# Kernel optimization log

Measured on AMD Instinct MI355X. Metric: run time of the kernel, lower is better.

Reference implementation:

```python
import jax, jax.numpy as jnp
import numpy as np

B, N, T, F_IN = 16, 1024, 12, 1
D_MODEL, D_K, D_V, H, K = 512, 32, 32, 3, 3
C = 32  # nb_chev_filter == nb_time_filter


def _ln(x, g, b, eps=1e-5):
    mu = jnp.mean(x, -1, keepdims=True)
    var = jnp.var(x, -1, keepdims=True)
    return (x - mu) * jax.lax.rsqrt(var + eps) * g + b


def _conv(x, w, b):
    y = jax.lax.conv_general_dilated(x, w, (1, 1), 'VALID',
                                     dimension_numbers=('NCHW', 'OIHW', 'NCHW'))
    return y + b[None, :, None, None]


def setup_inputs() -> dict:
    key = jax.random.key(0)
    ks = iter(jax.random.split(key, 40))
    rn = lambda s, sc=0.02: jax.random.normal(next(ks), s, jnp.float32) * sc
    return dict(
        x=rn((B, N, F_IN, T), 1.0),
        res_att=rn((B, F_IN, H, T, T), 0.1),
        pos_embed_T=rn((T, N)),
        gamma_T=jnp.ones((N,)), beta_T=jnp.zeros((N,)),
        WQ_t=rn((N, D_K * H)), WK_t=rn((N, D_K * H)), WV_t=rn((N, D_V * H)),
        fc_t=rn((H * D_V, N)),
        pre_conv_w=rn((D_MODEL, T, 1, F_IN)), pre_conv_b=rn((D_MODEL,)),
        pos_embed_S=rn((N, D_MODEL)),
        gamma_S=jnp.ones((D_MODEL,)), beta_S=jnp.zeros((D_MODEL,)),
        WQ_s=rn((D_MODEL, D_K * K)), WK_s=rn((D_MODEL, D_K * K)),
        cheb_polys=rn((K, N, N), 0.05),
        adj_pa=(jax.random.uniform(next(ks), (N, N)) < 0.01).astype(jnp.float32),
        cheb_mask=rn((K, N, N)),
        Theta=rn((K, F_IN, C), 0.1),
        gtu3_w=rn((2 * C, C, 1, 3)), gtu3_b=rn((2 * C,)),
        gtu5_w=rn((2 * C, C, 1, 5)), gtu5_b=rn((2 * C,)),
        gtu7_w=rn((2 * C, C, 1, 7)), gtu7_b=rn((2 * C,)),
        res_conv_w=rn((C, F_IN, 1, 1)), res_conv_b=rn((C,)),
        fcmy_w=rn((3 * T - 12, T)), fcmy_b=rn((T,)),
        gamma_f=jnp.ones((C,)), beta_f=jnp.zeros((C,)),
    )


def reference(x, res_att, pos_embed_T, gamma_T, beta_T, WQ_t, WK_t, WV_t, fc_t,
              pre_conv_w, pre_conv_b, pos_embed_S, gamma_S, beta_S, WQ_s, WK_s,
              cheb_polys, adj_pa, cheb_mask, Theta,
              gtu3_w, gtu3_b, gtu5_w, gtu5_b, gtu7_w, gtu7_b,
              res_conv_w, res_conv_b, fcmy_w, fcmy_b, gamma_f, beta_f):
    B_, N_, F_, T_ = x.shape
    # ---- temporal embedding (num_of_features == 1 branch): (B,F,T,N) ----
    TEmx = _ln(jnp.transpose(x, (0, 2, 3, 1)) + pos_embed_T[None, None], gamma_T, beta_T)

    # ---- temporal MHA with residual attention bias ----
    def heads(e, W, d):
        y = e @ W  # (B,F,T,H*d)
        return jnp.transpose(y.reshape(B_, F_, T_, H, d), (0, 1, 3, 2, 4))  # (B,F,H,T,d)
    Q, Kt, V = heads(TEmx, WQ_t, D_K), heads(TEmx, WK_t, D_K), heads(TEmx, WV_t, D_V)
    re_At = jnp.einsum('bfhqd,bfhkd->bfhqk', Q, Kt) / np.sqrt(D_K) + res_att
    attn = jax.nn.softmax(re_At, axis=-1)
    ctx = jnp.einsum('bfhqk,bfhkd->bfhqd', attn, V)
    ctx = jnp.transpose(ctx, (0, 1, 3, 2, 4)).reshape(B_, F_, T_, H * D_V)
    one_n, zero_n = jnp.ones((N_,), x.dtype), jnp.zeros((N_,), x.dtype)
    TATout = _ln(ctx @ fc_t + TEmx, one_n, zero_n)  # fresh LayerNorm(d_model) -> gamma=1, beta=0

    # ---- pre_conv: Conv2d(T, d_model, kernel=(1,F)) on (B,T,N,F); take last col ----
    x_TAt = jnp.einsum('btnf,dtf->bnd', jnp.transpose(TATout, (0, 2, 3, 1)),
                       pre_conv_w[:, :, 0, :]) + pre_conv_b  # (B,N,d_model)

    # ---- spatial embedding + spatial attention scores (no softmax) ----
    SEmx = _ln(x_TAt + pos_embed_S[None], gamma_S, beta_S)  # dropout = identity (eval)
    Qs = jnp.transpose((SEmx @ WQ_s).reshape(B_, N_, K, D_K), (0, 2, 1, 3))
    Ks = jnp.transpose((SEmx @ WK_s).reshape(B_, N_, K, D_K), (0, 2, 1, 3))
    STAt = jnp.einsum('bknd,bkmd->bknm', Qs, Ks) / np.sqrt(D_K)  # (B,K,N,N)

    # ---- Chebyshev graph conv weighted by spatial attention ----
    satt = jax.nn.softmax(STAt + (adj_pa[None] * cheb_mask)[None], axis=2)
    Tka = cheb_polys[None] * satt  # (B,K,N,N)
    rhs = jnp.einsum('bkmn,bmft->bknft', Tka, x)  # T_k_with_at^T @ x over all t
    spatial_gcn = jax.nn.relu(jnp.einsum('bknft,kfo->bnot', rhs, Theta))  # (B,N,C,T)

    # ---- gated temporal convs (GTU) ----
    X = jnp.transpose(spatial_gcn, (0, 2, 1, 3))  # (B,C,N,T)
    def gtu(w, b):
        y = _conv(X, w, b)
        return jnp.tanh(y[:, :C]) * jax.nn.sigmoid(y[:, C:])
    time_conv = jnp.concatenate([gtu(gtu3_w, gtu3_b), gtu(gtu5_w, gtu5_b),
                                 gtu(gtu7_w, gtu7_b)], axis=-1)  # (B,C,N,3T-12)
    time_conv = time_conv @ fcmy_w + fcmy_b  # (B,C,N,T)
    tco = jax.nn.relu(time_conv)  # num_of_features == 1 branch

    # ---- residual 1x1 conv + final LayerNorm over channel dim ----
    x_res = _conv(jnp.transpose(x, (0, 2, 1, 3)), res_conv_w, res_conv_b)  # (B,C,N,T)
    out = _ln(jnp.transpose(jax.nn.relu(x_res + tco), (0, 3, 2, 1)), gamma_f, beta_f)
    out = jnp.transpose(out, (0, 2, 3, 1))  # (B,N,C,T)
    return out, re_At
```

## Files before the change

### kernel.cpp

```cpp
#include <hip/hip_runtime.h>
#include <hip/hip_bf16.h>
#include <math.h>

#define B_ 16
#define N_ 1024
#define T_ 12
#define DM_ 512
#define H_ 3
#define K_ 3
#define C_ 32
#define RSQRT_DK 0.17677669529663687f

typedef __attribute__((ext_vector_type(8))) short bf16x8;
typedef __attribute__((ext_vector_type(4))) float f32x4;

__device__ __forceinline__ ushort f2bf(float f) {
  uint u = __float_as_uint(f);
  return (ushort)((u + 0x7FFF + ((u >> 16) & 1)) >> 16);
}
__device__ __forceinline__ float bf2f(ushort h) {
  return __uint_as_float(((uint)h) << 16);
}

__global__ void k1_temporal_ln(const float* __restrict__ x, const float* __restrict__ posT,
                               const float* __restrict__ gT, const float* __restrict__ bT,
                               float* __restrict__ TEmx) {
  int row = blockIdx.x;
  int b = row / T_, t = row - b * T_;
  __shared__ float red[256], red2[256];
  float v[4]; float s = 0.f, s2 = 0.f;
  for (int i = 0; i < 4; ++i) {
    int n = threadIdx.x + (i << 8);
    float val = x[(b * N_ + n) * T_ + t] + posT[t * N_ + n];
    v[i] = val; s += val; s2 += val * val;
  }
  red[threadIdx.x] = s; red2[threadIdx.x] = s2;
  __syncthreads();
  for (int off = 128; off > 0; off >>= 1) {
    if (threadIdx.x < off) { red[threadIdx.x] += red[threadIdx.x + off]; red2[threadIdx.x] += red2[threadIdx.x + off]; }
    __syncthreads();
  }
  float mu = red[0] * (1.f / N_);
  float rs = rsqrtf(red2[0] * (1.f / N_) - mu * mu + 1e-5f);
  for (int i = 0; i < 4; ++i) {
    int n = threadIdx.x + (i << 8);
    TEmx[row * N_ + n] = (v[i] - mu) * rs * gT[n] + bT[n];
  }
}

__global__ __launch_bounds__(256) void k2_qkv(const float* __restrict__ TEmx,
                       const float* __restrict__ WQ, const float* __restrict__ WK,
                       const float* __restrict__ WV, float* __restrict__ part) {
  int kc = blockIdx.x, row = blockIdx.y;
  __shared__ float e[256];
  int tid = threadIdx.x;
  e[tid] = TEmx[row * N_ + kc * 256 + tid];
  __syncthreads();
  for (int col = tid; col < 288; col += 256) {
    int which = col / 96, j = col - which * 96;
    const float* W = (which == 0) ? WQ : ((which == 1) ? WK : WV);
    const float* Wp = W + (size_t)(kc * 256) * 96 + j;
    float acc = 0.f;
    #pragma unroll 8
    for (int n = 0; n < 256; ++n) acc += e[n] * Wp[n * 96];
    part[(row * 4 + kc) * 288 + col] = acc;
  }
}

__global__ void k3a_attn(const float* __restrict__ part, const float* __restrict__ res_att,
                         float* __restrict__ reAt_out, float* __restrict__ ctx) {
  int b = blockIdx.x;
  __shared__ float q_l[T_ * 288];
  __shared__ float s_l[H_ * T_ * T_];
  for (int i = threadIdx.x; i < T_ * 288; i += 256) {
    int t = i / 288, col = i - t * 288;
    const float* pr = &part[(size_t)((b * T_ + t) * 4) * 288 + col];
    q_l[i] = pr[0] + pr[288] + pr[576] + pr[864];
  }
  __syncthreads();
  for (int idx = threadIdx.x; idx < H_ * T_ * T_; idx += 256) {
    int h = idx / 144, r = idx - h * 144, qi = r / 12, ki = r - qi * 12;
    float acc = 0.f;
    #pragma unroll
    for (int d = 0; d < 32; ++d)
      acc += q_l[qi * 288 + h * 32 + d] * q_l[ki * 288 + 96 + h * 32 + d];
    float sv = acc * RSQRT_DK + res_att[(b * H_ + h) * 144 + qi * 12 + ki];
    s_l[idx] = sv;
    reAt_out[(b * H_ + h) * 144 + qi * 12 + ki] = sv;
  }
  __syncthreads();
  if (threadIdx.x < 36) {
    int h = threadIdx.x / 12, qi = threadIdx.x - h * 12;
    float mx = -1e30f;
    for (int ki = 0; ki < 12; ++ki) mx = fmaxf(mx, s_l[h * 144 + qi * 12 + ki]);
    float sum = 0.f;
    for (int ki = 0; ki < 12; ++ki) { float p = __expf(s_l[h * 144 + qi * 12 + ki] - mx); s_l[h * 144 + qi * 12 + ki] = p; sum += p; }
    float inv = 1.f / sum;
    for (int ki = 0; ki < 12; ++ki) s_l[h * 144 + qi * 12 + ki] *= inv;
  }
  __syncthreads();
  for (int idx = threadIdx.x; idx < T_ * 96; idx += 256) {
    int qi = idx / 96, hd = idx - qi * 96, h = hd >> 5, d = hd & 31;
    float acc = 0.f;
    for (int ki = 0; ki < 12; ++ki)
      acc += s_l[h * 144 + qi * 12 + ki] * q_l[ki * 288 + 192 + h * 32 + d];
    ctx[(b * T_ + qi) * 96 + hd] = acc;
  }
}

__global__ __launch_bounds__(1024) void k3b_tat(const float* __restrict__ ctx,
                        const float* __restrict__ fc_t,
                        const float* __restrict__ TEmx, float* __restrict__ TAT) {
  int row = blockIdx.x;
  __shared__ float c_l[96];
  __shared__ float red[16], red2[16];
  int tid = threadIdx.x;
  if (tid < 96) c_l[tid] = ctx[row * 96 + tid];
  __syncthreads();
  float acc = TEmx[row * N_ + tid];
  #pragma unroll 12
  for (int j = 0; j < 96; ++j) acc = fmaf(c_l[j], fc_t[j * N_ + tid], acc);
  float s = acc, s2 = acc * acc;
  #pragma unroll
  for (int off = 32; off > 0; off >>= 1) {
    s  += __shfl_xor(s, off);
    s2 += __shfl_xor(s2, off);
  }
  int w = tid >> 6;
  if ((tid & 63) == 0) { red[w] = s; red2[w] = s2; }
  __syncthreads();
  float ts = 0.f, ts2 = 0.f;
  #pragma unroll
  for (int i = 0; i < 16; ++i) { ts += red[i]; ts2 += red2[i]; }
  float mu = ts * (1.f / N_);
  float rs = rsqrtf(ts2 * (1.f / N_) - mu * mu + 1e-5f);
  TAT[row * N_ + tid] = (acc - mu) * rs;
}

__global__ __launch_bounds__(256) void k4_preconv_ln(const float* __restrict__ TAT, const float* __restrict__ pcw,
                              const float* __restrict__ pcb, const float* __restrict__ posS,
                              const float* __restrict__ gS, const float* __restrict__ bS,
                              float* __restrict__ SEmx) {
  int wid = blockIdx.x * 4 + (threadIdx.x >> 6);
  int b = wid >> 10, n = wid & 1023;
  int lane = threadIdx.x & 63;
  float tc[12];
  #pragma unroll
  for (int t = 0; t < 12; ++t) tc[t] = TAT[(b * T_ + t) * N_ + n];
  float v[8]; float s = 0.f, s2 = 0.f;
  #pragma unroll
  for (int i = 0; i < 8; ++i) {
    int d = lane + (i << 6);
    const float4* pw = (const float4*)&pcw[d * 12];
    float4 w0 = pw[0], w1 = pw[1], w2 = pw[2];
    float acc = pcb[d];
    acc += tc[0] * w0.x + tc[1] * w0.y + tc[2] * w0.z + tc[3] * w0.w;
    acc += tc[4] * w1.x + tc[5] * w1.y + tc[6] * w1.z + tc[7] * w1.w;
    acc += tc[8] * w2.x + tc[9] * w2.y + tc[10] * w2.z + tc[11] * w2.w;
    acc += posS[(size_t)n * DM_ + d];
    v[i] = acc; s += acc; s2 += acc * acc;
  }
  #pragma unroll
  for (int off = 1; off < 64; off <<= 1) {
    s  += __shfl_xor(s, off);
    s2 += __shfl_xor(s2, off);
  }
  float mu = s * (1.f / DM_);
  float rs = rsqrtf(s2 * (1.f / DM_) - mu * mu + 1e-5f);
  #pragma unroll
  for (int i = 0; i < 8; ++i) {
    int d = lane + (i << 6);
    SEmx[(size_t)wid * DM_ + d] = (v[i] - mu) * rs * gS[d] + bS[d];
  }
}

__global__ void k5_pre(const float* __restrict__ WQs, const float* __restrict__ WKs,
                       ushort* __restrict__ wpre) {
  int idx = blockIdx.x * 256 + threadIdx.x;
  int k = idx / 192, col = idx - k * 192;
  float v = (col < 96) ? WQs[k * 96 + col] : WKs[k * 96 + (col - 96)];
  wpre[col * 512 + k] = f2bf(v);
}

__global__ __launch_bounds__(256) void k5_qks(const float* __restrict__ SEmx,
                                              const ushort* __restrict__ wpre,
                                              __hip_bfloat16* __restrict__ Qs,
                                              __hip_bfloat16* __restrict__ Ks) {
  int b = blockIdx.y, n0 = blockIdx.x * 32;
  __shared__ __align__(16) ushort SE_h[32 * 520];
  int tid = threadIdx.x;
  for (int idx = tid; idx < 4096; idx += 256) {
    int r = idx >> 7, cq = idx & 127;
    float4 v = *(const float4*)&SEmx[((size_t)((b << 10) + n0 + r)) * DM_ + cq * 4];
    uint lo = (uint)f2bf(v.x) | ((uint)f2bf(v.y) << 16);
    uint hi = (uint)f2bf(v.z) | ((uint)f2bf(v.w) << 16);
    *(uint2*)&SE_h[r * 520 + cq * 4] = make_uint2(lo, hi);
  }
  __syncthreads();

  int w = tid >> 6, lane = tid & 63, quad = lane >> 4, c16 = lane & 15;
  f32x4 acc[3][2];
  #pragma unroll
  for (int mi = 0; mi < 3; ++mi)
    #pragma unroll
    for (int nt = 0; nt < 2; ++nt) acc[mi][nt] = (f32x4){0.f, 0.f, 0.f, 0.f};

  for (int ks = 0; ks < 16; ++ks) {
    bf16x8 Bf0 = *(const bf16x8*)&SE_h[(0 * 16 + c16) * 520 + ks * 32 + quad * 8];
    bf16x8 Bf1 = *(const bf16x8*)&SE_h[(1 * 16 + c16) * 520 + ks * 32 + quad * 8];
    #pragma unroll
    for (int mi = 0; mi < 3; ++mi) {
      int m = (w * 3 + mi) * 16 + c16;
      bf16x8 Af = *(const bf16x8*)&wpre[m * 512 + ks * 32 + quad * 8];
      acc[mi][0] = __builtin_amdgcn_mfma_f32_16x16x32_bf16(Af, Bf0, acc[mi][0], 0, 0, 0);
      acc[mi][1] = __builtin_amdgcn_mfma_f32_16x16x32_bf16(Af, Bf1, acc[mi][1], 0, 0, 0);
    }
  }
  #pragma unroll
  for (int mi = 0; mi < 3; ++mi) {
    int mb = (w * 3 + mi) * 16;
    #pragma unroll
    for (int nt = 0; nt < 2; ++nt) {
      int node = n0 + nt * 16 + c16;
      #pragma unroll
      for (int r = 0; r < 4; ++r) {
        int m = mb + quad * 4 + r;
        int j = (m < 96) ? m : m - 96;
        int kk = j >> 5, dd = j & 31;
        __hip_bfloat16* o = (m < 96) ? Qs : Ks;
        o[(((b * K_ + kk) * N_) + node) * 32 + dd] = __float2bfloat16(acc[mi][nt][r]);
      }
    }
  }
}

__global__ void k6_pre(const float* __restrict__ adj, const float* __restrict__ mask,
                       const float* __restrict__ cheb, uint* __restrict__ pk) {
  int idx = blockIdx.x * 256 + threadIdx.x;
  int mn = idx & (N_ * N_ - 1);
  uint lo = f2bf(adj[mn] * mask[idx]);
  uint hi = f2bf(cheb[idx]);
  pk[idx] = lo | (hi << 16);
}

__global__ __launch_bounds__(256) void k6_spatial(
    const __hip_bfloat16* __restrict__ Qs, const __hip_bfloat16* __restrict__ Ks,
    const uint* __restrict__ pk, const float* __restrict__ x,
    float* __restrict__ rhs) {
  const int b  = blockIdx.x;
  const int k  = blockIdx.y;
  const int n0 = blockIdx.z * 32;
  const ushort* Qb = (const ushort*)(Qs + (size_t)((b * K_ + k) * N_) * 32);
  const ushort* Kb = (const ushort*)(Ks + (size_t)((b * K_ + k) * N_) * 32);
  const uint* pkk = pk + (size_t)k * (N_ * N_);
  const float* xb = x + b * N_ * T_;

  __shared__ float wmu[4][32], well[4][32];
  __shared__ float wacc[4][32][12];

  const int tid  = threadIdx.x;
  const int w    = tid >> 6, lane = tid & 63;
  const int quad = lane >> 4, c16 = lane & 15;

  bf16x8 bfr0 = *(const bf16x8*)(Kb + (size_t)(n0 + c16) * 32 + quad * 8);
  bf16x8 bfr1 = *(const bf16x8*)(Kb + (size_t)(n0 + 16 + c16) * 32 + quad * 8);

  float mu0 = -1e30f, mu1 = -1e30f, el0 = 0.f, el1 = 0.f;
  float acc0[12], acc1[12];
  #pragma unroll
  for (int t = 0; t < 12; ++t) { acc0[t] = 0.f; acc1[t] = 0.f; }

  for (int s = 0; s < 16; ++s) {
    const int m0 = s * 64 + w * 16;
    bf16x8 af = *(const bf16x8*)(Qb + (size_t)(m0 + c16) * 32 + quad * 8);
    f32x4 z = {0.f, 0.f, 0.f, 0.f};
    f32x4 sc0 = __builtin_amdgcn_mfma_f32_16x16x32_bf16(af, bfr0, z, 0, 0, 0);
    f32x4 sc1 = __builtin_amdgcn_mfma_f32_16x16x32_bf16(af, bfr1, z, 0, 0, 0);

    const int mrow = m0 + quad * 4;
    float sv0[4], sv1[4], ch0[4], ch1[4];
    #pragma unroll
    for (int r = 0; r < 4; ++r) {
      uint p2 = pkk[(size_t)(mrow + r) * N_ + n0 + c16];
      uint q2 = pkk[(size_t)(mrow + r) * N_ + n0 + 16 + c16];
      sv0[r] = sc0[r] * RSQRT_DK + __uint_as_float(p2 << 16);
      ch0[r] = __uint_as_float(p2 & 0xFFFF0000u);
      sv1[r] = sc1[r] * RSQRT_DK + __uint_as_float(q2 << 16);
      ch1[r] = __uint_as_float(q2 & 0xFFFF0000u);
    }
    float cm0 = fmaxf(fmaxf(sv0[0], sv0[1]), fmaxf(sv0[2], sv0[3]));
    float cm1 = fmaxf(fmaxf(sv1[0], sv1[1]), fmaxf(sv1[2], sv1[3]));
    cm0 = fmaxf(cm0, __shfl_xor(cm0, 16)); cm0 = fmaxf(cm0, __shfl_xor(cm0, 32));
    cm1 = fmaxf(cm1, __shfl_xor(cm1, 16)); cm1 = fmaxf(cm1, __shfl_xor(cm1, 32));
    float nm0 = fmaxf(mu0, cm0), nm1 = fmaxf(mu1, cm1);
    float f0 = __expf(mu0 - nm0), f1 = __expf(mu1 - nm1);
    mu0 = nm0; mu1 = nm1;
    el0 *= f0; el1 *= f1;
    #pragma unroll
    for (int t = 0; t < 12; ++t) { acc0[t] *= f0; acc1[t] *= f1; }

    float p0[4], p1[4];
    #pragma unroll
    for (int r = 0; r < 4; ++r) {
      p0[r] = __expf(sv0[r] - mu0); el0 += p0[r]; p0[r] *= ch0[r];
      p1[r] = __expf(sv1[r] - mu1); el1 += p1[r]; p1[r] *= ch1[r];
    }
    #pragma unroll
    for (int r = 0; r < 4; ++r) {
      const float4* xr = (const float4*)(xb + (size_t)(mrow + r) * 12);
      float4 xA = xr[0], xB = xr[1], xC = xr[2];
      float xv[12] = {xA.x, xA.y, xA.z, xA.w, xB.x, xB.y, xB.z, xB.w,
                      xC.x, xC.y, xC.z, xC.w};
      float px0 = p0[r], px1 = p1[r];
      #pragma unroll
      for (int t = 0; t < 12; ++t) {
        acc0[t] = fmaf(px0, xv[t], acc0[t]);
        acc1[t] = fmaf(px1, xv[t], acc1[t]);
      }
    }
  }

  #pragma unroll
  for (int off = 16; off <= 32; off <<= 1) {
    el0 += __shfl_xor(el0, off);
    el1 += __shfl_xor(el1, off);
    #pragma unroll
    for (int t = 0; t < 12; ++t) {
      acc0[t] += __shfl_xor(acc0[t], off);
      acc1[t] += __shfl_xor(acc1[t], off);
    }
  }
  if (quad == 0) {
    wmu[w][c16] = mu0; well[w][c16] = el0;
    #pragma unroll
    for (int t = 0; t < 12; ++t) wacc[w][c16][t] = acc0[t];
  } else if (quad == 1) {
    wmu[w][16 + c16] = mu1; well[w][16 + c16] = el1;
    #pragma unroll
    for (int t = 0; t < 12; ++t) wacc[w][16 + c16][t] = acc1[t];
  }
  __syncthreads();
  if (tid < 384) {
    int n = tid / 12, t = tid - n * 12;
    float m0v = wmu[0][n], m1v = wmu[1][n], m2v = wmu[2][n], m3v = wmu[3][n];
    float gm = fmaxf(fmaxf(m0v, m1v), fmaxf(m2v, m3v));
    float e0 = __expf(m0v - gm), e1 = __expf(m1v - gm);
    float e2 = __expf(m2v - gm), e3 = __expf(m3v - gm);
    float den = well[0][n] * e0 + well[1][n] * e1 + well[2][n] * e2 + well[3][n] * e3;
    float num = wacc[0][n][t] * e0 + wacc[1][n][t] * e1 +
                wacc[2][n][t] * e2 + wacc[3][n][t] * e3;
    rhs[((size_t)(b * K_ + k) * N_ + n0 + n) * 12 + t] = num / den;
  }
}

template<int KS, int JV, int JB>
__device__ __forceinline__ void conv_mfma(const ushort* X_th, const ushort* wl_h,
                                          ushort* tc_h, const float* bias0,
                                          int mp, int ntg, int quad, int c16) {
  f32x4 accA[3], accB[3];
  #pragma unroll
  for (int i = 0; i < 3; ++i) { accA[i] = (f32x4){0.f,0.f,0.f,0.f}; accB[i] = (f32x4){0.f,0.f,0.f,0.f}; }
  #pragma unroll
  for (int dt = 0; dt < KS; ++dt) {
    bf16x8 A0 = *(const bf16x8*)&wl_h[dt * 2560 + (mp * 16 + c16) * 40 + quad * 8];
    bf16x8 A1 = *(const bf16x8*)&wl_h[dt * 2560 + ((mp + 2) * 16 + c16) * 40 + quad * 8];
    #pragma unroll
    for (int i = 0; i < 3; ++i) {
      int nt = ntg * 3 + i;
      int j = nt >> 1, sh = nt & 1;
      if (j < JV) {
        bf16x8 Bf = *(const bf16x8*)&X_th[(sh * 16 + c16) * 584 + (j + dt) * 32 + quad * 8];
        accA[i] = __builtin_amdgcn_mfma_f32_16x16x32_bf16(A0, Bf, accA[i], 0, 0, 0);
        accB[i] = __builtin_amdgcn_mfma_f32_16x16x32_bf16(A1, Bf, accB[i], 0, 0, 0);
      }
    }
  }
  #pragma unroll
  for (int i = 0; i < 3; ++i) {
    int nt = ntg * 3 + i, j = nt >> 1, sh = nt & 1;
    if (j < JV) {
      int s = sh * 16 + c16;
      #pragma unroll
      for (int r = 0; r < 4; ++r) {
        int cc = mp * 16 + quad * 4 + r;
        int sx = ((s & 15) << 1) ^ ((cc & 4) << 3) ^ ((cc & 8) >> 1);
        float a = accA[i][r] + bias0[cc];
        float g = accB[i][r] + bias0[cc + 32];
        float e2a = __expf(2.f * a);
        float th = 1.f - 2.f / (e2a + 1.f);
        float sg = 1.f / (1.f + __expf(-g));
        tc_h[((s * 32 + cc) * 32 + (JB + j)) ^ sx] = f2bf(th * sg);
      }
    }
  }
}

__global__ __launch_bounds__(1024) void k8_fused(
                       const float* __restrict__ rhs, const float* __restrict__ Theta,
                       const float* __restrict__ x, const float* __restrict__ rw,
                       const float* __restrict__ rb,
                       const float* __restrict__ w3, const float* __restrict__ b3,
                       const float* __restrict__ w5, const float* __restrict__ b5,
                       const float* __restrict__ w7, const float* __restrict__ b7,
                       const float* __restrict__ fw, const float* __restrict__ fb,
                       const float* __restrict__ gf, const float* __restrict__ bf,
                       float* __restrict__ out) {
  int bn0 = blockIdx.x * 32;
  int b = bn0 >> 10, n0 = bn0 & 1023;

  __shared__ __align__(16) char uR[73216];
  ushort* X_th = (ushort*)uR;
  ushort* wl_h = (ushort*)(uR + 37376);
  float*  v_l  = (float*)uR;
  __shared__ __align__(16) ushort tc_h[1024 * 32];
  __shared__ float rhs_l[32 * 36];
  __shared__ float Th_l[96];
  __shared__ float xr_l[32 * 12];
  __shared__ float fw_l[288];
  __shared__ float fb_l[12];
  __shared__ float bias_l[3][64];
  __shared__ float rw_l[32], rb_l[32], gf_l[32], bf_l[32];
  __shared__ float stm[384], str[384];

  int tid = threadIdx.x;
  int w = tid >> 6, lane = tid & 63, quad = lane >> 4, c16 = lane & 15;
  int mp = w & 1, ntg = w >> 1;
  int c = (tid >> 3) & 31;
  int site = (tid & 7) | ((tid >> 8) << 3);

  for (int idx = tid; idx < 1152; idx += 1024) {
    int s = idx / 36, r = idx - s * 36, k = r / 12, t = r - k * 12;
    rhs_l[idx] = rhs[((size_t)(b * 3 + k) * N_ + n0 + s) * 12 + t];
  }
  if (tid < 384) xr_l[tid] = x[(size_t)(b * N_ + n0) * 12 + tid];
  if (tid < 96) Th_l[tid] = Theta[tid];
  if (tid < 288) fw_l[tid] = fw[tid];
  if (tid < 12) fb_l[tid] = fb[tid];
  if (tid < 64) { bias_l[0][tid] = b3[tid]; bias_l[1][tid] = b5[tid]; bias_l[2][tid] = b7[tid]; }
  if (tid >= 64 && tid < 96)  rw_l[tid - 64] = rw[tid - 64];
  if (tid >= 96 && tid < 128) rb_l[tid - 96] = rb[tid - 96];
  if (tid >= 128 && tid < 160) gf_l[tid - 128] = gf[tid - 128];
  if (tid >= 160 && tid < 192) bf_l[tid - 160] = bf[tid - 160];
  for (int idx = tid; idx < 64 * 32 * 3; idx += 1024) {
    int co = idx / 96, r2 = idx - co * 96, ic = r2 / 3, dt = r2 - ic * 3;
    wl_h[dt * 2560 + co * 40 + ic] = f2bf(w3[idx]);
  }
  __syncthreads();

  {
    float th0 = Th_l[c], th1 = Th_l[32 + c], th2 = Th_l[64 + c];
    const float* rs_ = &rhs_l[site * 36];
    ushort* xo = &X_th[site * 584 + c];
    #pragma unroll
    for (int t = 0; t < 12; ++t) {
      float a = rs_[t] * th0 + rs_[12 + t] * th1 + rs_[24 + t] * th2;
      xo[t * 32] = f2bf(fmaxf(a, 0.f));
    }
  }
  for (int idx = tid; idx < 32 * 6 * 32; idx += 1024) {
    int s = idx / 192, r2 = idx - s * 192, tt = r2 >> 5, ic = r2 & 31;
    X_th[s * 584 + (12 + tt) * 32 + ic] = 0;
  }
  __syncthreads();

  conv_mfma<3, 10, 0>(X_th, wl_h, tc_h, &bias_l[0][0], mp, ntg, quad, c16);
  __syncthreads();
  for (int idx = tid; idx < 64 * 32 * 5; idx += 1024) {
    int co = idx / 160, r2 = idx - co * 160, ic = r2 / 5, dt = r2 - ic * 5;
    wl_h[dt * 2560 + co * 40 + ic] = f2bf(w5[idx]);
  }
  __syncthreads();
  conv_mfma<5, 8, 10>(X_th, wl_h, tc_h, &bias_l[1][0], mp, ntg, quad, c16);
  __syncthreads();
  for (int idx = tid; idx < 64 * 32 * 7; idx += 1024) {
    int co = idx / 224, r2 = idx - co * 224, ic = r2 / 7, dt = r2 - ic * 7;
    wl_h[dt * 2560 + co * 40 + ic] = f2bf(w7[idx]);
  }
  __syncthreads();
  conv_mfma<7, 6, 18>(X_th, wl_h, tc_h, &bias_l[2][0], mp, ntg, quad, c16);
  __syncthreads();

  float tcv[24];
  {
    int rb2 = (site * 32 + c) * 32;
    int sxr = ((site & 15) << 1) ^ ((c & 4) << 3) ^ ((c & 8) >> 1);
    #pragma unroll
    for (int j = 0; j < 24; ++j)
      tcv[j] = __uint_as_float(((uint)tc_h[(rb2 + j) ^ sxr]) << 16);
  }
  float o[12];
  #pragma unroll
  for (int t = 0; t < 12; ++t) o[t] = fb_l[t];
  #pragma unroll
  for (int j = 0; j < 24; ++j) {
    const float4* fp = (const float4*)&fw_l[j * 12];
    float4 f0 = fp[0], f1 = fp[1], f2 = fp[2];
    float fr[12] = {f0.x, f0.y, f0.z, f0.w, f1.x, f1.y, f1.z, f1.w, f2.x, f2.y, f2.z, f2.w};
    #pragma unroll
    for (int t = 0; t < 12; ++t) o[t] = fmaf(tcv[j], fr[t], o[t]);
  }

  float v[12];
  {
    float rwc = rw_l[c], rbc = rb_l[c];
    const float* xs = &xr_l[site * 12];
    float* vo = &v_l[site * 391 + c * 12];
    #pragma unroll
    for (int t = 0; t < 12; ++t) {
      float xres = xs[t] * rwc + rbc;
      v[t] = fmaxf(xres + fmaxf(o[t], 0.f), 0.f);
      vo[t] = v[t];
    }
  }
  __syncthreads();
  if (tid < 384) {
    int s = tid / 12, t = tid - s * 12;
    float sm = 0.f, s2 = 0.f;
    #pragma unroll 8
    for (int cc = 0; cc < 32; ++cc) {
      float u = v_l[s * 391 + cc * 12 + t];
      sm += u; s2 += u * u;
    }
    float m = sm * (1.f / 32.f);
    stm[tid] = m;
    str[tid] = rsqrtf(s2 * (1.f / 32.f) - m * m + 1e-5f);
  }
  __syncthreads();
  {
    float gfc = gf_l[c], bfc = bf_l[c];
    const float* sm_ = &stm[site * 12];
    const float* sr_ = &str[site * 12];
    float q[12];
    #pragma unroll
    for (int t = 0; t < 12; ++t) q[t] = (v[t] - sm_[t]) * sr_[t] * gfc + bfc;
    float* op = &out[(size_t)(bn0 + site) * 384 + c * 12];
    ((float4*)op)[0] = make_float4(q[0], q[1], q[2], q[3]);
    ((float4*)op)[1] = make_float4(q[4], q[5], q[6], q[7]);
    ((float4*)op)[2] = make_float4(q[8], q[9], q[10], q[11]);
  }
}

extern "C" void kernel_launch(void* const* d_in, const int* in_sizes, int n_in,
                              void* d_out, int out_size, void* d_ws, size_t ws_size,
                              hipStream_t stream) {
  const float* x       = (const float*)d_in[0];
  const float* res_att = (const float*)d_in[1];
  const float* posT    = (const float*)d_in[2];
  const float* gT      = (const float*)d_in[3];
  const float* bT      = (const float*)d_in[4];
  const float* WQt     = (const float*)d_in[5];
  const float* WKt     = (const float*)d_in[6];
  const float* WVt     = (const float*)d_in[7];
  const float* fct     = (const float*)d_in[8];
  const float* pcw     = (const float*)d_in[9];
  const float* pcb     = (const float*)d_in[10];
  const float* posS    = (const float*)d_in[11];
  const float* gS      = (const float*)d_in[12];
  const float* bS      = (const float*)d_in[13];
  const float* WQs     = (const float*)d_in[14];
  const float* WKs     = (const float*)d_in[15];
  const float* cheb    = (const float*)d_in[16];
  const float* adj     = (const float*)d_in[17];
  const float* mask    = (const float*)d_in[18];
  const float* Theta   = (const float*)d_in[19];
  const float* w3      = (const float*)d_in[20];
  const float* b3      = (const float*)d_in[21];
  const float* w5      = (const float*)d_in[22];
  const float* b5      = (const float*)d_in[23];
  const float* w7      = (const float*)d_in[24];
  const float* b7      = (const float*)d_in[25];
  const float* rw      = (const float*)d_in[26];
  const float* rb      = (const float*)d_in[27];
  const float* fw      = (const float*)d_in[28];
  const float* fb      = (const float*)d_in[29];
  const float* gf      = (const float*)d_in[30];
  const float* bf      = (const float*)d_in[31];

  float* ws = (float*)d_ws;
  float* TEmx = ws;
  float* qkv  = TEmx + 196608;
  float* ctx  = qkv + 55296;
  float* TAT  = ctx + 18432;
  float* SEmx = TAT + 196608;
  float* Qsf  = SEmx + 8388608;
  float* Ksf  = Qsf + 1572864;
  float* rhs  = Ksf + 1572864;
  ushort* wpre = (ushort*)(rhs + 589824);
  float* part = SEmx;

  __hip_bfloat16* Qh = (__hip_bfloat16*)Qsf;
  __hip_bfloat16* Kh = (__hip_bfloat16*)Ksf;
  uint* pk = (uint*)SEmx;

  float* out  = (float*)d_out;
  float* reAt = out + 6291456;

  k5_pre<<<(DM_ * 192) / 256, 256, 0, stream>>>(WQs, WKs, wpre);
  k1_temporal_ln<<<B_ * T_, 256, 0, stream>>>(x, posT, gT, bT, TEmx);
  k2_qkv<<<dim3(4, B_ * T_), 256, 0, stream>>>(TEmx, WQt, WKt, WVt, part);
  k3a_attn<<<B_, 256, 0, stream>>>(part, res_att, reAt, ctx);
  k3b_tat<<<B_ * T_, 1024, 0, stream>>>(ctx, fct, TEmx, TAT);
  k4_preconv_ln<<<B_ * N_ / 4, 256, 0, stream>>>(TAT, pcw, pcb, posS, gS, bS, SEmx);
  k5_qks<<<dim3(N_ / 32, B_), 256, 0, stream>>>(SEmx, wpre, Qh, Kh);
  k6_pre<<<(K_ * N_ * N_) / 256, 256, 0, stream>>>(adj, mask, cheb, pk);
  k6_spatial<<<dim3(B_, K_, N_ / 32), 256, 0, stream>>>(Qh, Kh, pk, x, rhs);
  k8_fused<<<B_ * N_ / 32, 1024, 0, stream>>>(rhs, Theta, x, rw, rb,
                                              w3, b3, w5, b5, w7, b7, fw, fb, gf, bf, out);
}
```

Before: 363.7 us.

## Precompute bf16 GTU conv weights globally and split temporal attention per head

A new k8_pre kernel converts the three GTU conv weight tensors to bf16 once, in MFMA-friendly layout, into an unused workspace slot. k8_fused then loads the A fragments straight from global memory instead of converting and staging weights in LDS before each conv. This removes the per-block conversion loops and several barriers, and shrinks the shared-memory buffer. The cost is weight fetches through the cache hierarchy inside the MFMA loop. Separately, k3a_attn now runs one block per (batch, head), launching three times as many blocks with smaller LDS tiles.

Result: faster. 329.2 us (-9.5%).

```diff
diff --git a/kernel.cpp b/kernel.cpp
--- a/kernel.cpp
+++ b/kernel.cpp
@@ -67,44 +67,46 @@
   }
 }
 
-__global__ void k3a_attn(const float* __restrict__ part, const float* __restrict__ res_att,
+__global__ __launch_bounds__(256) void k3a_attn(const float* __restrict__ part, const float* __restrict__ res_att,
                          float* __restrict__ reAt_out, float* __restrict__ ctx) {
-  int b = blockIdx.x;
-  __shared__ float q_l[T_ * 288];
-  __shared__ float s_l[H_ * T_ * T_];
-  for (int i = threadIdx.x; i < T_ * 288; i += 256) {
-    int t = i / 288, col = i - t * 288;
+  int bh = blockIdx.x;
+  int b = bh / 3, h = bh - b * 3;
+  __shared__ float q_l[3 * T_ * 32];
+  __shared__ float s_l[T_ * T_];
+  int tid = threadIdx.x;
+  for (int i = tid; i < 1152; i += 256) {
+    int sec = i / 384, r = i - sec * 384, t = r >> 5, d = r & 31;
+    int col = sec * 96 + h * 32 + d;
     const float* pr = &part[(size_t)((b * T_ + t) * 4) * 288 + col];
     q_l[i] = pr[0] + pr[288] + pr[576] + pr[864];
   }
   __syncthreads();
-  for (int idx = threadIdx.x; idx < H_ * T_ * T_; idx += 256) {
-    int h = idx / 144, r = idx - h * 144, qi = r / 12, ki = r - qi * 12;
+  if (tid < 144) {
+    int qi = tid / 12, ki = tid - qi * 12;
     float acc = 0.f;
     #pragma unroll
     for (int d = 0; d < 32; ++d)
-      acc += q_l[qi * 288 + h * 32 + d] * q_l[ki * 288 + 96 + h * 32 + d];
-    float sv = acc * RSQRT_DK + res_att[(b * H_ + h) * 144 + qi * 12 + ki];
-    s_l[idx] = sv;
-    reAt_out[(b * H_ + h) * 144 + qi * 12 + ki] = sv;
-  }
-  __syncthreads();
-  if (threadIdx.x < 36) {
-    int h = threadIdx.x / 12, qi = threadIdx.x - h * 12;
+      acc += q_l[qi * 32 + d] * q_l[384 + ki * 32 + d];
+    float sv = acc * RSQRT_DK + res_att[(size_t)bh * 144 + tid];
+    s_l[tid] = sv;
+    reAt_out[(size_t)bh * 144 + tid] = sv;
+  }
+  __syncthreads();
+  if (tid < 12) {
     float mx = -1e30f;
-    for (int ki = 0; ki < 12; ++ki) mx = fmaxf(mx, s_l[h * 144 + qi * 12 + ki]);
+    for (int ki = 0; ki < 12; ++ki) mx = fmaxf(mx, s_l[tid * 12 + ki]);
     float sum = 0.f;
-    for (int ki = 0; ki < 12; ++ki) { float p = __expf(s_l[h * 144 + qi * 12 + ki] - mx); s_l[h * 144 + qi * 12 + ki] = p; sum += p; }
+    for (int ki = 0; ki < 12; ++ki) { float p = __expf(s_l[tid * 12 + ki] - mx); s_l[tid * 12 + ki] = p; sum += p; }
     float inv = 1.f / sum;
-    for (int ki = 0; ki < 12; ++ki) s_l[h * 144 + qi * 12 + ki] *= inv;
-  }
-  __syncthreads();
-  for (int idx = threadIdx.x; idx < T_ * 96; idx += 256) {
-    int qi = idx / 96, hd = idx - qi * 96, h = hd >> 5, d = hd & 31;
+    for (int ki = 0; ki < 12; ++ki) s_l[tid * 12 + ki] *= inv;
+  }
+  __syncthreads();
+  for (int i = tid; i < 384; i += 256) {
+    int qi = i >> 5, d = i & 31;
     float acc = 0.f;
     for (int ki = 0; ki < 12; ++ki)
-      acc += s_l[h * 144 + qi * 12 + ki] * q_l[ki * 288 + 192 + h * 32 + d];
-    ctx[(b * T_ + qi) * 96 + hd] = acc;
+      acc += s_l[qi * 12 + ki] * q_l[768 + ki * 32 + d];
+    ctx[(size_t)(b * T_ + qi) * 96 + h * 32 + d] = acc;
   }
 }
 
@@ -180,6 +182,23 @@
   int k = idx / 192, col = idx - k * 192;
   float v = (col < 96) ? WQs[k * 96 + col] : WKs[k * 96 + (col - 96)];
   wpre[col * 512 + k] = f2bf(v);
+}
+
+__global__ void k8_pre(const float* __restrict__ w3, const float* __restrict__ w5,
+                       const float* __restrict__ w7, ushort* __restrict__ wg) {
+  int idx = blockIdx.x * 256 + threadIdx.x;
+  if (idx < 6144) {
+    int dt = idx / 2048, rem = idx - dt * 2048, co = rem >> 5, ic = rem & 31;
+    wg[idx] = f2bf(w3[(co * 32 + ic) * 3 + dt]);
+  } else if (idx < 16384) {
+    int ds = idx - 6144;
+    int dt = ds / 2048, rem = ds - dt * 2048, co = rem >> 5, ic = rem & 31;
+    wg[idx] = f2bf(w5[(co * 32 + ic) * 5 + dt]);
+  } else if (idx < 30720) {
+    int ds = idx - 16384;
+    int dt = ds / 2048, rem = ds - dt * 2048, co = rem >> 5, ic = rem & 31;
+    wg[idx] = f2bf(w7[(co * 32 + ic) * 7 + dt]);
+  }
 }
 
 __global__ __launch_bounds__(256) void k5_qks(const float* __restrict__ SEmx,
@@ -353,37 +372,36 @@
   }
 }
 
-template<int KS, int JV, int JB>
-__device__ __forceinline__ void conv_mfma(const ushort* X_th, const ushort* wl_h,
-                                          ushort* tc_h, const float* bias0,
-                                          int mp, int ntg, int quad, int c16) {
+template<int KS, int JV, int JB, int WOFF>
+__device__ __forceinline__ void conv_mfma_g(const ushort* X_th, const ushort* __restrict__ wg,
+                                            ushort* tc_h, const float* bias0,
+                                            int mp, int ntg, int quad, int c16) {
   f32x4 accA[3], accB[3];
   #pragma unroll
   for (int i = 0; i < 3; ++i) { accA[i] = (f32x4){0.f,0.f,0.f,0.f}; accB[i] = (f32x4){0.f,0.f,0.f,0.f}; }
   #pragma unroll
   for (int dt = 0; dt < KS; ++dt) {
-    bf16x8 A0 = *(const bf16x8*)&wl_h[dt * 2560 + (mp * 16 + c16) * 40 + quad * 8];
-    bf16x8 A1 = *(const bf16x8*)&wl_h[dt * 2560 + ((mp + 2) * 16 + c16) * 40 + quad * 8];
+    bf16x8 A0 = *(const bf16x8*)&wg[WOFF + (dt * 64 + mp * 16 + c16) * 32 + quad * 8];
+    bf16x8 A1 = *(const bf16x8*)&wg[WOFF + (dt * 64 + (mp + 2) * 16 + c16) * 32 + quad * 8];
     #pragma unroll
     for (int i = 0; i < 3; ++i) {
       int nt = ntg * 3 + i;
       int j = nt >> 1, sh = nt & 1;
-      if (j < JV) {
-        bf16x8 Bf = *(const bf16x8*)&X_th[(sh * 16 + c16) * 584 + (j + dt) * 32 + quad * 8];
-        accA[i] = __builtin_amdgcn_mfma_f32_16x16x32_bf16(A0, Bf, accA[i], 0, 0, 0);
-        accB[i] = __builtin_amdgcn_mfma_f32_16x16x32_bf16(A1, Bf, accB[i], 0, 0, 0);
-      }
-    }
-  }
+      bf16x8 Bf = *(const bf16x8*)&X_th[(sh * 16 + c16) * 584 + (j + dt) * 32 + quad * 8];
+      accA[i] = __builtin_amdgcn_mfma_f32_16x16x32_bf16(A0, Bf, accA[i], 0, 0, 0);
+      accB[i] = __builtin_amdgcn_mfma_f32_16x16x32_bf16(A1, Bf, accB[i], 0, 0, 0);
+    }
+  }
+  int sxq = ((quad & 1) << 5) ^ ((quad & 2) << 1);
   #pragma unroll
   for (int i = 0; i < 3; ++i) {
     int nt = ntg * 3 + i, j = nt >> 1, sh = nt & 1;
     if (j < JV) {
       int s = sh * 16 + c16;
+      int sx = ((s & 15) << 1) ^ sxq;
       #pragma unroll
       for (int r = 0; r < 4; ++r) {
         int cc = mp * 16 + quad * 4 + r;
-        int sx = ((s & 15) << 1) ^ ((cc & 4) << 3) ^ ((cc & 8) >> 1);
         float a = accA[i][r] + bias0[cc];
         float g = accB[i][r] + bias0[cc + 32];
         float e2a = __expf(2.f * a);
@@ -399,18 +417,17 @@
                        const float* __restrict__ rhs, const float* __restrict__ Theta,
                        const float* __restrict__ x, const float* __restrict__ rw,
                        const float* __restrict__ rb,
-                       const float* __restrict__ w3, const float* __restrict__ b3,
-                       const float* __restrict__ w5, const float* __restrict__ b5,
-                       const float* __restrict__ w7, const float* __restrict__ b7,
+                       const ushort* __restrict__ wg,
+                       const float* __restrict__ b3, const float* __restrict__ b5,
+                       const float* __restrict__ b7,
                        const float* __restrict__ fw, const float* __restrict__ fb,
                        const float* __restrict__ gf, const float* __restrict__ bf,
                        float* __restrict__ out) {
   int bn0 = blockIdx.x * 32;
   int b = bn0 >> 10, n0 = bn0 & 1023;
 
-  __shared__ __align__(16) char uR[73216];
+  __shared__ __align__(16) char uR[50176];
   ushort* X_th = (ushort*)uR;
-  ushort* wl_h = (ushort*)(uR + 37376);
   float*  v_l  = (float*)uR;
   __shared__ __align__(16) ushort tc_h[1024 * 32];
   __shared__ float rhs_l[32 * 36];
@@ -441,10 +458,6 @@
   if (tid >= 96 && tid < 128) rb_l[tid - 96] = rb[tid - 96];
   if (tid >= 128 && tid < 160) gf_l[tid - 128] = gf[tid - 128];
   if (tid >= 160 && tid < 192) bf_l[tid - 160] = bf[tid - 160];
-  for (int idx = tid; idx < 64 * 32 * 3; idx += 1024) {
-    int co = idx / 96, r2 = idx - co * 96, ic = r2 / 3, dt = r2 - ic * 3;
-    wl_h[dt * 2560 + co * 40 + ic] = f2bf(w3[idx]);
-  }
   __syncthreads();
 
   {
@@ -463,21 +476,9 @@
   }
   __syncthreads();
 
-  conv_mfma<3, 10, 0>(X_th, wl_h, tc_h, &bias_l[0][0], mp, ntg, quad, c16);
-  __syncthreads();
-  for (int idx = tid; idx < 64 * 32 * 5; idx += 1024) {
-    int co = idx / 160, r2 = idx - co * 160, ic = r2 / 5, dt = r2 - ic * 5;
-    wl_h[dt * 2560 + co * 40 + ic] = f2bf(w5[idx]);
-  }
-  __syncthreads();
-  conv_mfma<5, 8, 10>(X_th, wl_h, tc_h, &bias_l[1][0], mp, ntg, quad, c16);
-  __syncthreads();
-  for (int idx = tid; idx < 64 * 32 * 7; idx += 1024) {
-    int co = idx / 224, r2 = idx - co * 224, ic = r2 / 7, dt = r2 - ic * 7;
-    wl_h[dt * 2560 + co * 40 + ic] = f2bf(w7[idx]);
-  }
-  __syncthreads();
-  conv_mfma<7, 6, 18>(X_th, wl_h, tc_h, &bias_l[2][0], mp, ntg, quad, c16);
+  conv_mfma_g<3, 10, 0,      0>(X_th, wg, tc_h, &bias_l[0][0], mp, ntg, quad, c16);
+  conv_mfma_g<5, 8, 10,   6144>(X_th, wg, tc_h, &bias_l[1][0], mp, ntg, quad, c16);
+  conv_mfma_g<7, 6, 18,  16384>(X_th, wg, tc_h, &bias_l[2][0], mp, ntg, quad, c16);
   __syncthreads();
 
   float tcv[24];
@@ -586,6 +587,7 @@
   float* Ksf  = Qsf + 1572864;
   float* rhs  = Ksf + 1572864;
   ushort* wpre = (ushort*)(rhs + 589824);
+  ushort* wg   = (ushort*)qkv;
   float* part = SEmx;
 
   __hip_bfloat16* Qh = (__hip_bfloat16*)Qsf;
@@ -596,14 +598,15 @@
   float* reAt = out + 6291456;
 
   k5_pre<<<(DM_ * 192) / 256, 256, 0, stream>>>(WQs, WKs, wpre);
+  k8_pre<<<120, 256, 0, stream>>>(w3, w5, w7, wg);
   k1_temporal_ln<<<B_ * T_, 256, 0, stream>>>(x, posT, gT, bT, TEmx);
   k2_qkv<<<dim3(4, B_ * T_), 256, 0, stream>>>(TEmx, WQt, WKt, WVt, part);
-  k3a_attn<<<B_, 256, 0, stream>>>(part, res_att, reAt, ctx);
+  k3a_attn<<<B_ * H_, 256, 0, stream>>>(part, res_att, reAt, ctx);
   k3b_tat<<<B_ * T_, 1024, 0, stream>>>(ctx, fct, TEmx, TAT);
   k4_preconv_ln<<<B_ * N_ / 4, 256, 0, stream>>>(TAT, pcw, pcb, posS, gS, bS, SEmx);
   k5_qks<<<dim3(N_ / 32, B_), 256, 0, stream>>>(SEmx, wpre, Qh, Kh);
   k6_pre<<<(K_ * N_ * N_) / 256, 256, 0, stream>>>(adj, mask, cheb, pk);
   k6_spatial<<<dim3(B_, K_, N_ / 32), 256, 0, stream>>>(Qh, Kh, pk, x, rhs);
   k8_fused<<<B_ * N_ / 32, 1024, 0, stream>>>(rhs, Theta, x, rw, rb,
-                                              w3, b3, w5, b5, w7, b7, fw, fb, gf, bf, out);
-}
+                                              wg, b3, b5, b7, fw, fb, gf, bf, out);
+}
```
